# Kernel optimization log

Hardware: AMD Instinct MI355X
Metric: run time of the kernel (lower is better)

Reference implementation:

```python
import jax, jax.numpy as jnp
import numpy as np

B, Q, KV = 4, 256, 1024
QS, KS, H, VS = 128, 128, 128, 256

def setup_inputs() -> dict:
    key = jax.random.key(0)
    ks = jax.random.split(key, 7)
    return {
        "queries": jax.random.normal(ks[0], (B, Q, QS), dtype=jnp.float32),
        "keys": jax.random.normal(ks[1], (B, KV, KS), dtype=jnp.float32),
        "values": jax.random.normal(ks[2], (B, KV, VS), dtype=jnp.float32),
        "valid_lens": jax.random.randint(ks[3], (B,), 0, KV, dtype=jnp.int64 if jax.config.read('jax_enable_x64') else jnp.int32),
        "Wq": jax.random.normal(ks[4], (QS, H), dtype=jnp.float32),
        "Wk": jax.random.normal(ks[5], (KS, H), dtype=jnp.float32),
        "wv": jax.random.normal(ks[6], (H,), dtype=jnp.float32),
    }

def reference(queries, keys, values, valid_lens, Wq, Wk, wv):
    # project: [B,Q,H], [B,KV,H]
    q = jnp.einsum('bqd,dh->bqh', queries, Wq)
    k = jnp.einsum('bkd,dh->bkh', keys, Wk)
    # additive scores: broadcast add -> tanh -> reduce with w_v  [B,Q,KV]
    feats = jnp.tanh(q[:, :, None, :] + k[:, None, :, :])  # [B,Q,KV,H]
    scores = jnp.einsum('bqkh,h->bqk', feats, wv)
    # masked softmax over KV with value -1e6 at masked slots
    mask = jnp.arange(scores.shape[-1])[None, None, :] < valid_lens[:, None, None]
    scores = jnp.where(mask, scores, -1e6)
    attn = jax.nn.softmax(scores, axis=-1)
    # weighted sum of values  [B,Q,VS]
    return jnp.einsum('bqk,bkv->bqv', attn, values)
```

## Files before the change

### kernel.cpp

```cpp
#include <hip/hip_runtime.h>

#define C2LOG2E 2.8853900817779268f
#define LOG2E   1.4426950408889634f

__device__ __forceinline__ float sig2(float x) {
    return __builtin_amdgcn_rcpf(__builtin_amdgcn_exp2f(x) + 1.0f);
}

__global__ __launch_bounds__(256) void proj_kernel(
    const float* __restrict__ q_in, const float* __restrict__ k_in,
    const float* __restrict__ Wq, const float* __restrict__ Wk,
    float* __restrict__ qc, float* __restrict__ kct)
{
    __shared__ __align__(16) float in_s[4][128];
    __shared__ float ts[128][4];
    int tid = threadIdx.x;
    int r0 = blockIdx.x * 4;
    int rl = tid >> 7;
    int d  = tid & 127;
    bool is_q = (r0 < 1024);
#pragma unroll
    for (int j = 0; j < 2; ++j) {
        int r = r0 + 2*j + rl;
        const float* src = is_q ? (q_in + (size_t)r*128)
                                : (k_in + (size_t)(r-1024)*128);
        in_s[2*j+rl][d] = src[d];
    }
    __syncthreads();
    const float* W = is_q ? Wq : Wk;
    const float4* x0p = (const float4*)in_s[rl];
    const float4* x1p = (const float4*)in_s[rl+2];
    float4 c0 = {0,0,0,0}, c1 = {0,0,0,0};
#pragma unroll 4
    for (int d4 = 0; d4 < 32; ++d4) {
        float4 x0 = x0p[d4], x1 = x1p[d4];
        float w0 = W[(4*d4+0)*128 + d];
        float w1 = W[(4*d4+1)*128 + d];
        float w2 = W[(4*d4+2)*128 + d];
        float w3 = W[(4*d4+3)*128 + d];
        c0.x = fmaf(x0.x, w0, c0.x); c0.y = fmaf(x0.y, w1, c0.y);
        c0.z = fmaf(x0.z, w2, c0.z); c0.w = fmaf(x0.w, w3, c0.w);
        c1.x = fmaf(x1.x, w0, c1.x); c1.y = fmaf(x1.y, w1, c1.y);
        c1.z = fmaf(x1.z, w2, c1.z); c1.w = fmaf(x1.w, w3, c1.w);
    }
    float a0 = ((c0.x+c0.y)+(c0.z+c0.w)) * C2LOG2E;
    float a1 = ((c1.x+c1.y)+(c1.z+c1.w)) * C2LOG2E;

    if (is_q) {
        qc[(size_t)(r0+rl)*128 + d]   = a0;
        qc[(size_t)(r0+rl+2)*128 + d] = a1;
    } else {
        ts[d][rl]   = a0;
        ts[d][rl+2] = a1;
        __syncthreads();
        if (tid < 128) {
            int kvg = r0 - 1024;
            int bb  = kvg >> 10;
            int kvb = kvg & 1023;
            int c   = kvb >> 6;
            int i   = kvb & 63;
            float4 t = *(const float4*)&ts[tid][0];
            *(float4*)&kct[(((size_t)(bb*16 + c))*128 + tid)*64 + i] = t;
        }
    }
}

__global__ __launch_bounds__(512, 4) void attn_kernel(
    const float* __restrict__ qc, const float* __restrict__ kct,
    const float* __restrict__ values, const int* __restrict__ valid_lens,
    const float* __restrict__ wv, float* __restrict__ out)
{
    __shared__ float2 e2_s[1024];
    __shared__ float4 po[8][2][64];
    __shared__ float  red_m[8][2], red_s[8][2];

    int tid  = threadIdx.x;
    int b    = blockIdx.y;
    int q0   = blockIdx.x * 2;
    int kvl  = tid & 511;
    int w    = tid >> 6;
    int lane = tid & 63;
    int vl   = valid_lens[b];

    const float4* qa4 = (const float4*)(qc + (size_t)(b*256 + q0)*128);
    const float4* qb4 = qa4 + 32;
    const float4* wv4 = (const float4*)wv;
    const float* p0 = kct + ((size_t)(b*16 + w))*128*64 + lane;
    const float* p1 = p0 + 8*128*64;

    bool act0 = (w*64 < vl);
    bool act1 = (512 + w*64 < vl);
    float a00=0.f, a01=0.f, a10=0.f, a11=0.f;

    if (act1) {
#pragma unroll 2
        for (int hb = 0; hb < 32; ++hb) {
            float4 qa = qa4[hb], qb = qb4[hb], wvv = wv4[hb];
            float k0a = p0[0], k0b = p0[64], k0c = p0[128], k0d = p0[192];
            float k1a = p1[0], k1b = p1[64], k1c = p1[128], k1d = p1[192];
            p0 += 256; p1 += 256;
            a00 = fmaf(wvv.x, sig2(qa.x + k0a), a00);
            a10 = fmaf(wvv.x, sig2(qb.x + k0a), a10);
            a01 = fmaf(wvv.x, sig2(qa.x + k1a), a01);
            a11 = fmaf(wvv.x, sig2(qb.x + k1a), a11);
            a00 = fmaf(wvv.y, sig2(qa.y + k0b), a00);
            a10 = fmaf(wvv.y, sig2(qb.y + k0b), a10);
            a01 = fmaf(wvv.y, sig2(qa.y + k1b), a01);
            a11 = fmaf(wvv.y, sig2(qb.y + k1b), a11);
            a00 = fmaf(wvv.z, sig2(qa.z + k0c), a00);
            a10 = fmaf(wvv.z, sig2(qb.z + k0c), a10);
            a01 = fmaf(wvv.z, sig2(qa.z + k1c), a01);
            a11 = fmaf(wvv.z, sig2(qb.z + k1c), a11);
            a00 = fmaf(wvv.w, sig2(qa.w + k0d), a00);
            a10 = fmaf(wvv.w, sig2(qb.w + k0d), a10);
            a01 = fmaf(wvv.w, sig2(qa.w + k1d), a01);
            a11 = fmaf(wvv.w, sig2(qb.w + k1d), a11);
        }
    } else if (act0) {
#pragma unroll 2
        for (int hb = 0; hb < 32; ++hb) {
            float4 qa = qa4[hb], qb = qb4[hb], wvv = wv4[hb];
            float k0a = p0[0], k0b = p0[64], k0c = p0[128], k0d = p0[192];
            p0 += 256;
            a00 = fmaf(wvv.x, sig2(qa.x + k0a), a00);
            a10 = fmaf(wvv.x, sig2(qb.x + k0a), a10);
            a00 = fmaf(wvv.y, sig2(qa.y + k0b), a00);
            a10 = fmaf(wvv.y, sig2(qb.y + k0b), a10);
            a00 = fmaf(wvv.z, sig2(qa.z + k0c), a00);
            a10 = fmaf(wvv.z, sig2(qb.z + k0c), a10);
            a00 = fmaf(wvv.w, sig2(qa.w + k0d), a00);
            a10 = fmaf(wvv.w, sig2(qb.w + k0d), a10);
        }
    }

    float s00 = (kvl       < vl) ? -2.f*a00 : -1e6f;
    float s10 = (kvl       < vl) ? -2.f*a10 : -1e6f;
    float s01 = (kvl + 512 < vl) ? -2.f*a01 : -1e6f;
    float s11 = (kvl + 512 < vl) ? -2.f*a11 : -1e6f;

    float m0 = fmaxf(s00, s01), m1 = fmaxf(s10, s11);
#pragma unroll
    for (int off = 32; off; off >>= 1) {
        m0 = fmaxf(m0, __shfl_xor(m0, off));
        m1 = fmaxf(m1, __shfl_xor(m1, off));
    }
    if (lane == 0) { red_m[w][0] = m0; red_m[w][1] = m1; }
    __syncthreads();
    m0 = red_m[0][0]; m1 = red_m[0][1];
#pragma unroll
    for (int ww = 1; ww < 8; ++ww) {
        m0 = fmaxf(m0, red_m[ww][0]);
        m1 = fmaxf(m1, red_m[ww][1]);
    }

    float e00 = __builtin_amdgcn_exp2f((s00 - m0) * LOG2E);
    float e10 = __builtin_amdgcn_exp2f((s10 - m1) * LOG2E);
    float e01 = __builtin_amdgcn_exp2f((s01 - m0) * LOG2E);
    float e11 = __builtin_amdgcn_exp2f((s11 - m1) * LOG2E);
    e2_s[kvl]       = make_float2(e00, e10);
    e2_s[kvl + 512] = make_float2(e01, e11);
    float l0 = e00 + e01, l1 = e10 + e11;
#pragma unroll
    for (int off = 32; off; off >>= 1) {
        l0 += __shfl_xor(l0, off);
        l1 += __shfl_xor(l1, off);
    }
    if (lane == 0) { red_s[w][0] = l0; red_s[w][1] = l1; }
    __syncthreads();
    float sum0 = red_s[0][0], sum1 = red_s[0][1];
#pragma unroll
    for (int ww = 1; ww < 8; ++ww) { sum0 += red_s[ww][0]; sum1 += red_s[ww][1]; }
    float inv0 = 1.0f / sum0, inv1 = 1.0f / sum1;

    int kv_end = (vl == 0) ? 1024 : vl;
    float4 ac0 = {0,0,0,0}, ac1 = {0,0,0,0};
    const float4* V4 = (const float4*)values + (size_t)b*1024*64 + lane;
#pragma unroll 2
    for (int kv = w; kv < kv_end; kv += 8) {
        float4 vv = V4[(size_t)kv*64];
        float2 ee = e2_s[kv];
        ac0.x = fmaf(ee.x, vv.x, ac0.x); ac0.y = fmaf(ee.x, vv.y, ac0.y);
        ac0.z = fmaf(ee.x, vv.z, ac0.z); ac0.w = fmaf(ee.x, vv.w, ac0.w);
        ac1.x = fmaf(ee.y, vv.x, ac1.x); ac1.y = fmaf(ee.y, vv.y, ac1.y);
        ac1.z = fmaf(ee.y, vv.z, ac1.z); ac1.w = fmaf(ee.y, vv.w, ac1.w);
    }
    po[w][0][lane] = ac0;
    po[w][1][lane] = ac1;
    __syncthreads();

    int qq = tid >> 8, col = tid & 255;
    const float* pp = (const float*)po;
    float r = 0.f;
#pragma unroll
    for (int ww = 0; ww < 8; ++ww) r += pp[(ww*2 + qq)*256 + col];
    float inv = qq ? inv1 : inv0;
    out[((size_t)(b*256 + q0 + qq))*256 + col] = r * inv;
}

extern "C" void kernel_launch(void* const* d_in, const int* in_sizes, int n_in,
                              void* d_out, int out_size, void* d_ws, size_t ws_size,
                              hipStream_t stream)
{
    const float* queries = (const float*)d_in[0];
    const float* keys    = (const float*)d_in[1];
    const float* values  = (const float*)d_in[2];
    const int*   vlens   = (const int*)d_in[3];
    const float* Wq      = (const float*)d_in[4];
    const float* Wk      = (const float*)d_in[5];
    const float* wv      = (const float*)d_in[6];
    float* out = (float*)d_out;

    float* qc  = (float*)d_ws;
    float* kct = qc + 4*256*128;

    proj_kernel<<<1280, 256, 0, stream>>>(queries, keys, Wq, Wk, qc, kct);
    attn_kernel<<<dim3(128, 4), 512, 0, stream>>>(qc, kct, values, vlens, wv, out);
}
```

Baseline: 100.8 us.

## Process four queries per attention block and eight rows per projection thread

```diff
diff --git a/kernel.cpp b/kernel.cpp
--- a/kernel.cpp
+++ b/kernel.cpp
@@ -7,194 +7,194 @@
     return __builtin_amdgcn_rcpf(__builtin_amdgcn_exp2f(x) + 1.0f);
 }
 
-__global__ __launch_bounds__(256) void proj_kernel(
+__global__ __launch_bounds__(128) void proj_kernel(
     const float* __restrict__ q_in, const float* __restrict__ k_in,
     const float* __restrict__ Wq, const float* __restrict__ Wk,
     float* __restrict__ qc, float* __restrict__ kct)
 {
-    __shared__ __align__(16) float in_s[4][128];
-    __shared__ float ts[128][4];
-    int tid = threadIdx.x;
-    int r0 = blockIdx.x * 4;
-    int rl = tid >> 7;
-    int d  = tid & 127;
-    bool is_q = (r0 < 1024);
-#pragma unroll
-    for (int j = 0; j < 2; ++j) {
-        int r = r0 + 2*j + rl;
-        const float* src = is_q ? (q_in + (size_t)r*128)
-                                : (k_in + (size_t)(r-1024)*128);
-        in_s[2*j+rl][d] = src[d];
-    }
-    __syncthreads();
+    int h   = threadIdx.x;
+    int blk = blockIdx.x;
+    bool is_q = (blk < 128);
+    int r0 = is_q ? blk*8 : (blk-128)*8;
+    const float* X = (is_q ? q_in : k_in) + (size_t)r0*128;
     const float* W = is_q ? Wq : Wk;
-    const float4* x0p = (const float4*)in_s[rl];
-    const float4* x1p = (const float4*)in_s[rl+2];
-    float4 c0 = {0,0,0,0}, c1 = {0,0,0,0};
+
+    float acc[8] = {0,0,0,0,0,0,0,0};
 #pragma unroll 4
     for (int d4 = 0; d4 < 32; ++d4) {
-        float4 x0 = x0p[d4], x1 = x1p[d4];
-        float w0 = W[(4*d4+0)*128 + d];
-        float w1 = W[(4*d4+1)*128 + d];
-        float w2 = W[(4*d4+2)*128 + d];
-        float w3 = W[(4*d4+3)*128 + d];
-        c0.x = fmaf(x0.x, w0, c0.x); c0.y = fmaf(x0.y, w1, c0.y);
-        c0.z = fmaf(x0.z, w2, c0.z); c0.w = fmaf(x0.w, w3, c0.w);
-        c1.x = fmaf(x1.x, w0, c1.x); c1.y = fmaf(x1.y, w1, c1.y);
-        c1.z = fmaf(x1.z, w2, c1.z); c1.w = fmaf(x1.w, w3, c1.w);
-    }
-    float a0 = ((c0.x+c0.y)+(c0.z+c0.w)) * C2LOG2E;
-    float a1 = ((c1.x+c1.y)+(c1.z+c1.w)) * C2LOG2E;
+        float w0 = W[(4*d4+0)*128 + h];
+        float w1 = W[(4*d4+1)*128 + h];
+        float w2 = W[(4*d4+2)*128 + h];
+        float w3 = W[(4*d4+3)*128 + h];
+#pragma unroll
+        for (int r = 0; r < 8; ++r) {
+            float4 xv = *(const float4*)(X + (size_t)r*128 + 4*d4);
+            acc[r] = fmaf(xv.x, w0,
+                     fmaf(xv.y, w1,
+                     fmaf(xv.z, w2,
+                     fmaf(xv.w, w3, acc[r]))));
+        }
+    }
+#pragma unroll
+    for (int r = 0; r < 8; ++r) acc[r] *= C2LOG2E;
 
     if (is_q) {
-        qc[(size_t)(r0+rl)*128 + d]   = a0;
-        qc[(size_t)(r0+rl+2)*128 + d] = a1;
+#pragma unroll
+        for (int r = 0; r < 8; ++r) qc[(size_t)(r0 + r)*128 + h] = acc[r];
     } else {
-        ts[d][rl]   = a0;
-        ts[d][rl+2] = a1;
-        __syncthreads();
-        if (tid < 128) {
-            int kvg = r0 - 1024;
-            int bb  = kvg >> 10;
-            int kvb = kvg & 1023;
-            int c   = kvb >> 6;
-            int i   = kvb & 63;
-            float4 t = *(const float4*)&ts[tid][0];
-            *(float4*)&kct[(((size_t)(bb*16 + c))*128 + tid)*64 + i] = t;
-        }
-    }
-}
-
-__global__ __launch_bounds__(512, 4) void attn_kernel(
+        int bb = r0 >> 10;
+        int c  = (r0 & 1023) >> 6;
+        int i0 = r0 & 63;
+        float* dst = kct + (((size_t)(bb*16 + c))*128 + h)*64 + i0;
+        *(float4*)dst       = make_float4(acc[0], acc[1], acc[2], acc[3]);
+        *(float4*)(dst + 4) = make_float4(acc[4], acc[5], acc[6], acc[7]);
+    }
+}
+
+__global__ __launch_bounds__(512, 2) void attn_kernel(
     const float* __restrict__ qc, const float* __restrict__ kct,
     const float* __restrict__ values, const int* __restrict__ valid_lens,
     const float* __restrict__ wv, float* __restrict__ out)
 {
-    __shared__ float2 e2_s[1024];
-    __shared__ float4 po[8][2][64];
-    __shared__ float  red_m[8][2], red_s[8][2];
+    __shared__ float4 e4_s[1024];
+    __shared__ float4 po[8][4][64];
+    __shared__ float  red_m[8][4], red_s[8][4];
 
     int tid  = threadIdx.x;
     int b    = blockIdx.y;
-    int q0   = blockIdx.x * 2;
-    int kvl  = tid & 511;
+    int q0   = blockIdx.x * 4;
     int w    = tid >> 6;
     int lane = tid & 63;
+    int kvl  = tid & 511;
     int vl   = valid_lens[b];
 
-    const float4* qa4 = (const float4*)(qc + (size_t)(b*256 + q0)*128);
-    const float4* qb4 = qa4 + 32;
+    const float4* q40 = (const float4*)(qc + (size_t)(b*256 + q0)*128);
     const float4* wv4 = (const float4*)wv;
-    const float* p0 = kct + ((size_t)(b*16 + w))*128*64 + lane;
-    const float* p1 = p0 + 8*128*64;
+    const float* p0 = kct + ((size_t)(b*16 + w))*8192 + lane;
+    const float* p1 = kct + ((size_t)(b*16 + w + 8))*8192 + lane;
 
     bool act0 = (w*64 < vl);
-    bool act1 = (512 + w*64 < vl);
-    float a00=0.f, a01=0.f, a10=0.f, a11=0.f;
+    bool act1 = ((w + 8)*64 < vl);
+    float a0[4] = {0,0,0,0}, a1[4] = {0,0,0,0};
 
     if (act1) {
-#pragma unroll 2
         for (int hb = 0; hb < 32; ++hb) {
-            float4 qa = qa4[hb], qb = qb4[hb], wvv = wv4[hb];
-            float k0a = p0[0], k0b = p0[64], k0c = p0[128], k0d = p0[192];
-            float k1a = p1[0], k1b = p1[64], k1c = p1[128], k1d = p1[192];
+            float4 wvv = wv4[hb];
+            float4 k0 = make_float4(p0[0], p0[64], p0[128], p0[192]);
+            float4 k1 = make_float4(p1[0], p1[64], p1[128], p1[192]);
             p0 += 256; p1 += 256;
-            a00 = fmaf(wvv.x, sig2(qa.x + k0a), a00);
-            a10 = fmaf(wvv.x, sig2(qb.x + k0a), a10);
-            a01 = fmaf(wvv.x, sig2(qa.x + k1a), a01);
-            a11 = fmaf(wvv.x, sig2(qb.x + k1a), a11);
-            a00 = fmaf(wvv.y, sig2(qa.y + k0b), a00);
-            a10 = fmaf(wvv.y, sig2(qb.y + k0b), a10);
-            a01 = fmaf(wvv.y, sig2(qa.y + k1b), a01);
-            a11 = fmaf(wvv.y, sig2(qb.y + k1b), a11);
-            a00 = fmaf(wvv.z, sig2(qa.z + k0c), a00);
-            a10 = fmaf(wvv.z, sig2(qb.z + k0c), a10);
-            a01 = fmaf(wvv.z, sig2(qa.z + k1c), a01);
-            a11 = fmaf(wvv.z, sig2(qb.z + k1c), a11);
-            a00 = fmaf(wvv.w, sig2(qa.w + k0d), a00);
-            a10 = fmaf(wvv.w, sig2(qb.w + k0d), a10);
-            a01 = fmaf(wvv.w, sig2(qa.w + k1d), a01);
-            a11 = fmaf(wvv.w, sig2(qb.w + k1d), a11);
+#pragma unroll
+            for (int q = 0; q < 4; ++q) {
+                float4 qv = q40[q*32 + hb];
+                a0[q] = fmaf(wvv.x, sig2(qv.x + k0.x), a0[q]);
+                a1[q] = fmaf(wvv.x, sig2(qv.x + k1.x), a1[q]);
+                a0[q] = fmaf(wvv.y, sig2(qv.y + k0.y), a0[q]);
+                a1[q] = fmaf(wvv.y, sig2(qv.y + k1.y), a1[q]);
+                a0[q] = fmaf(wvv.z, sig2(qv.z + k0.z), a0[q]);
+                a1[q] = fmaf(wvv.z, sig2(qv.z + k1.z), a1[q]);
+                a0[q] = fmaf(wvv.w, sig2(qv.w + k0.w), a0[q]);
+                a1[q] = fmaf(wvv.w, sig2(qv.w + k1.w), a1[q]);
+            }
         }
     } else if (act0) {
-#pragma unroll 2
         for (int hb = 0; hb < 32; ++hb) {
-            float4 qa = qa4[hb], qb = qb4[hb], wvv = wv4[hb];
-            float k0a = p0[0], k0b = p0[64], k0c = p0[128], k0d = p0[192];
+            float4 wvv = wv4[hb];
+            float4 k0 = make_float4(p0[0], p0[64], p0[128], p0[192]);
             p0 += 256;
-            a00 = fmaf(wvv.x, sig2(qa.x + k0a), a00);
-            a10 = fmaf(wvv.x, sig2(qb.x + k0a), a10);
-            a00 = fmaf(wvv.y, sig2(qa.y + k0b), a00);
-            a10 = fmaf(wvv.y, sig2(qb.y + k0b), a10);
-            a00 = fmaf(wvv.z, sig2(qa.z + k0c), a00);
-            a10 = fmaf(wvv.z, sig2(qb.z + k0c), a10);
-            a00 = fmaf(wvv.w, sig2(qa.w + k0d), a00);
-            a10 = fmaf(wvv.w, sig2(qb.w + k0d), a10);
+#pragma unroll
+            for (int q = 0; q < 4; ++q) {
+                float4 qv = q40[q*32 + hb];
+                a0[q] = fmaf(wvv.x, sig2(qv.x + k0.x), a0[q]);
+                a0[q] = fmaf(wvv.y, sig2(qv.y + k0.y), a0[q]);
+                a0[q] = fmaf(wvv.z, sig2(qv.z + k0.z), a0[q]);
+                a0[q] = fmaf(wvv.w, sig2(qv.w + k0.w), a0[q]);
+            }
         }
     }
 
-    float s00 = (kvl       < vl) ? -2.f*a00 : -1e6f;
-    float s10 = (kvl       < vl) ? -2.f*a10 : -1e6f;
-    float s01 = (kvl + 512 < vl) ? -2.f*a01 : -1e6f;
-    float s11 = (kvl + 512 < vl) ? -2.f*a11 : -1e6f;
-
-    float m0 = fmaxf(s00, s01), m1 = fmaxf(s10, s11);
-#pragma unroll
-    for (int off = 32; off; off >>= 1) {
-        m0 = fmaxf(m0, __shfl_xor(m0, off));
-        m1 = fmaxf(m1, __shfl_xor(m1, off));
-    }
-    if (lane == 0) { red_m[w][0] = m0; red_m[w][1] = m1; }
+    bool v0 = (kvl < vl), v1 = (kvl + 512 < vl);
+    float s0[4], s1[4], m[4];
+#pragma unroll
+    for (int q = 0; q < 4; ++q) {
+        s0[q] = v0 ? -2.f*a0[q] : -1e6f;
+        s1[q] = v1 ? -2.f*a1[q] : -1e6f;
+        m[q]  = fmaxf(s0[q], s1[q]);
+    }
+#pragma unroll
+    for (int off = 32; off; off >>= 1)
+#pragma unroll
+        for (int q = 0; q < 4; ++q) m[q] = fmaxf(m[q], __shfl_xor(m[q], off));
+    if (lane == 0) {
+#pragma unroll
+        for (int q = 0; q < 4; ++q) red_m[w][q] = m[q];
+    }
     __syncthreads();
-    m0 = red_m[0][0]; m1 = red_m[0][1];
-#pragma unroll
-    for (int ww = 1; ww < 8; ++ww) {
-        m0 = fmaxf(m0, red_m[ww][0]);
-        m1 = fmaxf(m1, red_m[ww][1]);
-    }
-
-    float e00 = __builtin_amdgcn_exp2f((s00 - m0) * LOG2E);
-    float e10 = __builtin_amdgcn_exp2f((s10 - m1) * LOG2E);
-    float e01 = __builtin_amdgcn_exp2f((s01 - m0) * LOG2E);
-    float e11 = __builtin_amdgcn_exp2f((s11 - m1) * LOG2E);
-    e2_s[kvl]       = make_float2(e00, e10);
-    e2_s[kvl + 512] = make_float2(e01, e11);
-    float l0 = e00 + e01, l1 = e10 + e11;
-#pragma unroll
-    for (int off = 32; off; off >>= 1) {
-        l0 += __shfl_xor(l0, off);
-        l1 += __shfl_xor(l1, off);
-    }
-    if (lane == 0) { red_s[w][0] = l0; red_s[w][1] = l1; }
+#pragma unroll
+    for (int q = 0; q < 4; ++q) {
+        m[q] = red_m[0][q];
+#pragma unroll
+        for (int ww = 1; ww < 8; ++ww) m[q] = fmaxf(m[q], red_m[ww][q]);
+    }
+
+    float e0[4], e1[4], l[4];
+#pragma unroll
+    for (int q = 0; q < 4; ++q) {
+        e0[q] = __builtin_amdgcn_exp2f((s0[q] - m[q]) * LOG2E);
+        e1[q] = __builtin_amdgcn_exp2f((s1[q] - m[q]) * LOG2E);
+        l[q]  = e0[q] + e1[q];
+    }
+    e4_s[kvl]       = make_float4(e0[0], e0[1], e0[2], e0[3]);
+    e4_s[kvl + 512] = make_float4(e1[0], e1[1], e1[2], e1[3]);
+#pragma unroll
+    for (int off = 32; off; off >>= 1)
+#pragma unroll
+        for (int q = 0; q < 4; ++q) l[q] += __shfl_xor(l[q], off);
+    if (lane == 0) {
+#pragma unroll
+        for (int q = 0; q < 4; ++q) red_s[w][q] = l[q];
+    }
     __syncthreads();
-    float sum0 = red_s[0][0], sum1 = red_s[0][1];
-#pragma unroll
-    for (int ww = 1; ww < 8; ++ww) { sum0 += red_s[ww][0]; sum1 += red_s[ww][1]; }
-    float inv0 = 1.0f / sum0, inv1 = 1.0f / sum1;
+    float inv[4];
+#pragma unroll
+    for (int q = 0; q < 4; ++q) {
+        float s = red_s[0][q];
+#pragma unroll
+        for (int ww = 1; ww < 8; ++ww) s += red_s[ww][q];
+        inv[q] = 1.0f / s;
+    }
 
     int kv_end = (vl == 0) ? 1024 : vl;
-    float4 ac0 = {0,0,0,0}, ac1 = {0,0,0,0};
+    float4 ac[4] = {{0,0,0,0},{0,0,0,0},{0,0,0,0},{0,0,0,0}};
     const float4* V4 = (const float4*)values + (size_t)b*1024*64 + lane;
 #pragma unroll 2
     for (int kv = w; kv < kv_end; kv += 8) {
         float4 vv = V4[(size_t)kv*64];
-        float2 ee = e2_s[kv];
-        ac0.x = fmaf(ee.x, vv.x, ac0.x); ac0.y = fmaf(ee.x, vv.y, ac0.y);
-        ac0.z = fmaf(ee.x, vv.z, ac0.z); ac0.w = fmaf(ee.x, vv.w, ac0.w);
-        ac1.x = fmaf(ee.y, vv.x, ac1.x); ac1.y = fmaf(ee.y, vv.y, ac1.y);
-        ac1.z = fmaf(ee.y, vv.z, ac1.z); ac1.w = fmaf(ee.y, vv.w, ac1.w);
-    }
-    po[w][0][lane] = ac0;
-    po[w][1][lane] = ac1;
+        float4 ee = e4_s[kv];
+        ac[0].x = fmaf(ee.x, vv.x, ac[0].x); ac[0].y = fmaf(ee.x, vv.y, ac[0].y);
+        ac[0].z = fmaf(ee.x, vv.z, ac[0].z); ac[0].w = fmaf(ee.x, vv.w, ac[0].w);
+        ac[1].x = fmaf(ee.y, vv.x, ac[1].x); ac[1].y = fmaf(ee.y, vv.y, ac[1].y);
+        ac[1].z = fmaf(ee.y, vv.z, ac[1].z); ac[1].w = fmaf(ee.y, vv.w, ac[1].w);
+        ac[2].x = fmaf(ee.z, vv.x, ac[2].x); ac[2].y = fmaf(ee.z, vv.y, ac[2].y);
+        ac[2].z = fmaf(ee.z, vv.z, ac[2].z); ac[2].w = fmaf(ee.z, vv.w, ac[2].w);
+        ac[3].x = fmaf(ee.w, vv.x, ac[3].x); ac[3].y = fmaf(ee.w, vv.y, ac[3].y);
+        ac[3].z = fmaf(ee.w, vv.z, ac[3].z); ac[3].w = fmaf(ee.w, vv.w, ac[3].w);
+    }
+#pragma unroll
+    for (int q = 0; q < 4; ++q) po[w][q][lane] = ac[q];
     __syncthreads();
 
-    int qq = tid >> 8, col = tid & 255;
+    int qq  = tid >> 7;
+    int col = (tid & 127) * 2;
     const float* pp = (const float*)po;
-    float r = 0.f;
-#pragma unroll
-    for (int ww = 0; ww < 8; ++ww) r += pp[(ww*2 + qq)*256 + col];
-    float inv = qq ? inv1 : inv0;
-    out[((size_t)(b*256 + q0 + qq))*256 + col] = r * inv;
+    float rx = 0.f, ry = 0.f;
+#pragma unroll
+    for (int ww = 0; ww < 8; ++ww) {
+        float2 p = *(const float2*)&pp[(ww*4 + qq)*256 + col];
+        rx += p.x; ry += p.y;
+    }
+    float iv = inv[qq];
+    *(float2*)&out[((size_t)(b*256 + q0 + qq))*256 + col] =
+        make_float2(rx * iv, ry * iv);
 }
 
 extern "C" void kernel_launch(void* const* d_in, const int* in_sizes, int n_in,
@@ -213,6 +213,6 @@
     float* qc  = (float*)d_ws;
     float* kct = qc + 4*256*128;
 
-    proj_kernel<<<1280, 256, 0, stream>>>(queries, keys, Wq, Wk, qc, kct);
-    attn_kernel<<<dim3(128, 4), 512, 0, stream>>>(qc, kct, values, vlens, wv, out);
-}
+    proj_kernel<<<640, 128, 0, stream>>>(queries, keys, Wq, Wk, qc, kct);
+    attn_kernel<<<dim3(64, 4), 512, 0, stream>>>(qc, kct, values, vlens, wv, out);
+}
```

New measurement: 118.0 us. 17.0% more time.
